# Optimization experiments

Measured on AMD Instinct MI355X. Metric: run time of the kernel, lower is better.

## Reference

```python
import jax, jax.numpy as jnp
import numpy as np

BN_EPS = 1e-5


def setup_inputs() -> dict:
    key = jax.random.key(0)
    k1, k2, k3 = jax.random.split(key, 3)
    B, IN, H, C = 65536, 784, 1024, 10
    x = jax.random.normal(k1, (B, IN), dtype=jnp.float32)
    # Kaiming-ish real-valued latent weights
    w1 = jax.random.normal(k2, (H, IN), dtype=jnp.float32) * 0.03
    w2 = jax.random.normal(k3, (C, H), dtype=jnp.float32) * 0.03
    gamma = jnp.ones((H,), dtype=jnp.float32)
    beta = jnp.zeros((H,), dtype=jnp.float32)
    return {"x": x, "w1": w1, "w2": w2, "gamma": gamma, "beta": beta}


def _bin_weight(w):
    # XNOR-Net weight binarization: per-output-row alpha * sign(w)
    alpha = jnp.mean(jnp.abs(w), axis=1, keepdims=True)  # [out, 1]
    return alpha * jnp.sign(w)


def reference(x, w1, w2, gamma, beta):
    x = x.reshape(x.shape[0], -1)                      # [B, 784]
    h = x @ _bin_weight(w1).T                          # [B, 1024]
    # BatchNorm1d, training mode: batch mean / biased variance
    mu = jnp.mean(h, axis=0)
    var = jnp.mean(jnp.square(h - mu), axis=0)
    h = gamma * (h - mu) * jax.lax.rsqrt(var + BN_EPS) + beta
    a = jnp.sign(h)                                    # binarized activation
    out = a @ _bin_weight(w2).T                        # [B, 10]
    return out
```

## Files before the change

### kernel.cpp

```cpp
#include <hip/hip_runtime.h>
#include <hip/hip_fp16.h>

#define BATCH   65536
#define IN_DIM  784
#define KPAD    800
#define K2      1600
#define KH      800
#define NSTEP   25
#define H_DIM   1024
#define C_DIM   10
#define BN_EPS  1e-5f

typedef _Float16 half8 __attribute__((ext_vector_type(8)));
typedef _Float16 half4 __attribute__((ext_vector_type(4)));
typedef float    f32x4 __attribute__((ext_vector_type(4)));

#if defined(__has_builtin)
#if __has_builtin(__builtin_amdgcn_global_load_lds)
#define HAVE_ASYNC 1
#endif
#endif
#ifndef HAVE_ASYNC
#define HAVE_ASYNC 0
#endif

__device__ __forceinline__ void stage16(const _Float16* g, _Float16* ldsBase, int lane) {
#if HAVE_ASYNC
  __builtin_amdgcn_global_load_lds((const __attribute__((address_space(1))) void*)g,
                                   (__attribute__((address_space(3))) void*)ldsBase,
                                   16, 0, 0);
#else
  *(half8*)(ldsBase + lane * 8) = *(const half8*)g;
#endif
}

__global__ __launch_bounds__(256) void split_x(const float* __restrict__ x,
                                               _Float16* __restrict__ X2) {
  const long tid = (long)blockIdx.x * 256 + threadIdx.x;
  const long row = tid / 100;
  const int  q   = (int)(tid - row * 100);
  const int  k   = q * 8;
  half8 hi = {}, lo = {};
  if (k < IN_DIM) {
#pragma unroll
    for (int h4 = 0; h4 < 2; ++h4) {
      const f32x4 v = *(const f32x4*)&x[row * IN_DIM + k + h4 * 4];
#pragma unroll
      for (int i = 0; i < 4; ++i) {
        const _Float16 h = (_Float16)v[i];
        hi[h4 * 4 + i] = h;
        lo[h4 * 4 + i] = (_Float16)(v[i] - (float)h);
      }
    }
  }
  _Float16* dst = X2 + row * K2 + k;
  *(half8*)dst = hi;
  *(half8*)(dst + KPAD) = lo;
}

__global__ __launch_bounds__(256) void prep_w(const float* __restrict__ w1,
                                              const float* __restrict__ w2,
                                              float* __restrict__ alpha1,
                                              _Float16* __restrict__ S2,
                                              float* __restrict__ bw2) {
  __shared__ float red[4];
  const int tid = threadIdx.x, lane = tid & 63, wave = tid >> 6;
  const int j = blockIdx.x;
  if (j < H_DIM) {
    const float* wr = w1 + (long)j * IN_DIM;
    float s = 0.f;
    for (int k = tid; k < IN_DIM; k += 256) s += fabsf(wr[k]);
#pragma unroll
    for (int off = 32; off > 0; off >>= 1) s += __shfl_xor(s, off, 64);
    if (lane == 0) red[wave] = s;
    __syncthreads();
    if (tid == 0) alpha1[j] = (red[0] + red[1] + red[2] + red[3]) * (1.f / IN_DIM);
    _Float16* dr = S2 + (long)j * KH;
    for (int k = tid; k < KH; k += 256) {
      const float v = (k < IN_DIM) ? wr[k] : 0.f;
      dr[k] = (_Float16)((v > 0.f) ? 1.f : ((v < 0.f) ? -1.f : 0.f));
    }
  } else {
    const int c = j - H_DIM;
    const float* wr = w2 + (long)c * H_DIM;
    float s = 0.f;
    for (int k = tid; k < H_DIM; k += 256) s += fabsf(wr[k]);
#pragma unroll
    for (int off = 32; off > 0; off >>= 1) s += __shfl_xor(s, off, 64);
    if (lane == 0) red[wave] = s;
    __syncthreads();
    const float alpha = (red[0] + red[1] + red[2] + red[3]) * (1.f / H_DIM);
    for (int k = tid; k < H_DIM; k += 256) {
      const float v = wr[k];
      const float sg = (v > 0.f) ? 1.f : ((v < 0.f) ? -1.f : 0.f);
      bw2[(long)c * H_DIM + k] = alpha * sg;
    }
  }
}

__global__ __launch_bounds__(512, 2) void gemm1(const _Float16* __restrict__ X2,
                                                const _Float16* __restrict__ S2,
                                                const float* __restrict__ alpha1,
                                                float* __restrict__ H,
                                                float* __restrict__ colsum,
                                                float* __restrict__ colsumsq) {
  __shared__ _Float16 lds[3 * 24576];
  const int tid  = threadIdx.x;
  const int lane = tid & 63;
  const int w    = tid >> 6;
  const int wr   = w >> 2;
  const int wc   = w & 3;

  const int b     = blockIdx.x;
  const int xcd   = b & 7;
  const int local = b >> 3;
  const long m0   = (long)(xcd * 32 + (local >> 2)) * 256;
  const int  n0   = (local & 3) * 256;

  const int c8 = ((lane & 3) ^ ((lane >> 3) & 3)) * 8;
  const _Float16* aG = X2 + (m0 + w * 32 + (lane >> 2)) * K2 + c8;
  const _Float16* bG = S2 + (long)(n0 + w * 32 + (lane >> 2)) * KH + c8;
  const int ldsW0 = (w * 32) * 32;
  const int ldsW1 = (w * 32 + 16) * 32;

  const int fr = lane & 15;
  const int kc = lane >> 4;
  const int cp = (kc ^ ((fr >> 1) & 3)) * 8;
  const int aoff = (wr * 128 + fr) * 32 + cp;
  const int boff = (wc * 64 + fr) * 32 + cp;

  f32x4 acc[8][4] = {};

#pragma unroll
  for (int kt = 0; kt < 2; ++kt) {
    _Float16* S = &lds[kt * 24576];
    const int k0 = kt * 32;
    stage16(aG + k0,                  S + ldsW0, lane);
    stage16(aG + 16 * K2 + k0,        S + ldsW1, lane);
    stage16(aG + KPAD + k0,           S + 8192 + ldsW0, lane);
    stage16(aG + KPAD + 16 * K2 + k0, S + 8192 + ldsW1, lane);
    stage16(bG + k0,                  S + 16384 + ldsW0, lane);
    stage16(bG + 16 * KH + k0,        S + 16384 + ldsW1, lane);
  }

  int scur = 0;
  int spre = 2;
  for (int t = 0; t < NSTEP; ++t) {
    _Float16* S = &lds[scur * 24576];
    const int ks = (t + 2 < NSTEP) ? (t + 2) * 32 : (NSTEP - 1) * 32;
    _Float16* P = &lds[spre * 24576];

    asm volatile("s_waitcnt vmcnt(6)" ::: "memory");
    __builtin_amdgcn_s_barrier();
    asm volatile("" ::: "memory");

    stage16(aG + ks,                  P + ldsW0, lane);
    stage16(aG + 16 * K2 + ks,        P + ldsW1, lane);
    stage16(aG + KPAD + ks,           P + 8192 + ldsW0, lane);
    stage16(aG + KPAD + 16 * K2 + ks, P + 8192 + ldsW1, lane);
    half8 af[8], bf[4];
#pragma unroll
    for (int ni = 0; ni < 4; ++ni) bf[ni] = *(const half8*)&S[16384 + boff + ni * 512];
#pragma unroll
    for (int mi = 0; mi < 8; ++mi) af[mi] = *(const half8*)&S[aoff + mi * 512];
    __builtin_amdgcn_s_setprio(1);
#pragma unroll
    for (int mi = 0; mi < 8; ++mi)
#pragma unroll
      for (int ni = 0; ni < 4; ++ni)
        acc[mi][ni] = __builtin_amdgcn_mfma_f32_16x16x32_f16(af[mi], bf[ni], acc[mi][ni], 0, 0, 0);
    __builtin_amdgcn_s_setprio(0);
    __builtin_amdgcn_s_barrier();

    stage16(bG + ks,           P + 16384 + ldsW0, lane);
    stage16(bG + 16 * KH + ks, P + 16384 + ldsW1, lane);
#pragma unroll
    for (int mi = 0; mi < 8; ++mi) af[mi] = *(const half8*)&S[8192 + aoff + mi * 512];
    __builtin_amdgcn_s_setprio(1);
#pragma unroll
    for (int mi = 0; mi < 8; ++mi)
#pragma unroll
      for (int ni = 0; ni < 4; ++ni)
        acc[mi][ni] = __builtin_amdgcn_mfma_f32_16x16x32_f16(af[mi], bf[ni], acc[mi][ni], 0, 0, 0);
    __builtin_amdgcn_s_setprio(0);

    scur = (scur == 2) ? 0 : scur + 1;
    spre = (spre == 2) ? 0 : spre + 1;
  }

  asm volatile("s_waitcnt vmcnt(0)" ::: "memory");

  const int rq = (lane >> 4) * 4;
#pragma unroll
  for (int ni = 0; ni < 4; ++ni) {
    const int col = n0 + wc * 64 + ni * 16 + fr;
    const float a1 = alpha1[col];
    float s = 0.f, q = 0.f;
#pragma unroll
    for (int mi = 0; mi < 8; ++mi) {
#pragma unroll
      for (int r = 0; r < 4; ++r) {
        const long row = m0 + wr * 128 + mi * 16 + rq + r;
        const float v = acc[mi][ni][r] * a1;
        H[row * H_DIM + col] = v;
        s += v;
        q += v * v;
      }
    }
    s += __shfl_xor(s, 16, 64);
    s += __shfl_xor(s, 32, 64);
    q += __shfl_xor(q, 16, 64);
    q += __shfl_xor(q, 32, 64);
    if ((lane >> 4) == 0) {
      atomicAdd(&colsum[col], s);
      atomicAdd(&colsumsq[col], q);
    }
  }
}

__global__ __launch_bounds__(256, 2) void final_k(const float* __restrict__ H,
                                                  const float* __restrict__ colsum,
                                                  const float* __restrict__ colsumsq,
                                                  const float* __restrict__ gamma,
                                                  const float* __restrict__ beta,
                                                  const float* __restrict__ bw2,
                                                  float* __restrict__ out) {
  const int tid = threadIdx.x, lane = tid & 63, wave = tid >> 6;
  f32x4 w2r[4][C_DIM];
  f32x4 csr[4], tsr[4];
#pragma unroll
  for (int c4 = 0; c4 < 4; ++c4) {
    const int col = c4 * 256 + lane * 4;
    const f32x4 s  = *(const f32x4*)&colsum[col];
    const f32x4 q  = *(const f32x4*)&colsumsq[col];
    const f32x4 g  = *(const f32x4*)&gamma[col];
    const f32x4 bt = *(const f32x4*)&beta[col];
    f32x4 c, t;
#pragma unroll
    for (int i = 0; i < 4; ++i) {
      const float mu  = s[i] * (1.f / BATCH);
      const float var = q[i] * (1.f / BATCH) - mu * mu;
      c[i] = g[i] * rsqrtf(var + BN_EPS);
      t[i] = bt[i] - c[i] * mu;
    }
    csr[c4] = c;
    tsr[c4] = t;
#pragma unroll
    for (int oc = 0; oc < C_DIM; ++oc)
      w2r[c4][oc] = *(const f32x4*)&bw2[oc * H_DIM + col];
  }

  const long wrow0 = ((long)blockIdx.x * 4 + wave) * 8;
#pragma unroll 1
  for (int r = 0; r < 8; ++r) {
    const long row = wrow0 + r;
    const float* hr = H + row * H_DIM;
    f32x4 h[4];
#pragma unroll
    for (int c4 = 0; c4 < 4; ++c4) h[c4] = *(const f32x4*)&hr[c4 * 256 + lane * 4];
    float p[C_DIM] = {};
#pragma unroll
    for (int c4 = 0; c4 < 4; ++c4) {
      f32x4 a;
#pragma unroll
      for (int i = 0; i < 4; ++i) {
        const float hv = h[c4][i] * csr[c4][i] + tsr[c4][i];
        a[i] = (hv > 0.f) ? 1.f : ((hv < 0.f) ? -1.f : 0.f);
      }
#pragma unroll
      for (int oc = 0; oc < C_DIM; ++oc) {
        const f32x4 wv = w2r[c4][oc];
        p[oc] += a[0] * wv[0] + a[1] * wv[1] + a[2] * wv[2] + a[3] * wv[3];
      }
    }
#pragma unroll
    for (int oc = 0; oc < C_DIM; ++oc) {
#pragma unroll
      for (int off = 32; off > 0; off >>= 1) p[oc] += __shfl_xor(p[oc], off, 64);
    }
    if (lane == 0) {
#pragma unroll
      for (int oc = 0; oc < C_DIM; ++oc) out[row * C_DIM + oc] = p[oc];
    }
  }
}

extern "C" void kernel_launch(void* const* d_in, const int* in_sizes, int n_in,
                              void* d_out, int out_size, void* d_ws, size_t ws_size,
                              hipStream_t stream) {
  const float* x     = (const float*)d_in[0];
  const float* w1    = (const float*)d_in[1];
  const float* w2    = (const float*)d_in[2];
  const float* gamma = (const float*)d_in[3];
  const float* beta  = (const float*)d_in[4];
  float* out = (float*)d_out;

  char* ws = (char*)d_ws;
  _Float16* X2     = (_Float16*)(ws + 0);
  float*    H      = (float*)  (ws + 209715200LL);
  _Float16* S2     = (_Float16*)(ws + 478150656LL);
  float*    BW2    = (float*)  (ws + 481427456LL);
  float*    ALPHA1 = (float*)  (ws + 481468416LL);
  float*    COLS   = (float*)  (ws + 481472512LL);
  float*    COLQ   = (float*)  (ws + 481476608LL);

  hipMemsetAsync(COLS, 0, 2 * H_DIM * sizeof(float), stream);
  split_x<<<(BATCH * 100) / 256, 256, 0, stream>>>(x, X2);
  prep_w<<<H_DIM + C_DIM, 256, 0, stream>>>(w1, w2, ALPHA1, S2, BW2);
  gemm1<<<1024, 512, 0, stream>>>(X2, S2, ALPHA1, H, COLS, COLQ);
  final_k<<<BATCH / 32, 256, 0, stream>>>(H, COLS, COLQ, gamma, beta, BW2, out);
}
```

Baseline: 606.5 us.

## Fuse fp16 hi/lo split of x into GEMM1 staging and drop memset launch

Removes the separate split_x kernel and its 200MB intermediate X2 buffer. GEMM1 now loads fp32 x directly, converts it to fp16 hi/lo pairs in registers and writes them into swizzled LDS, while still staging the weight tiles asynchronously. The column-sum zeroing moves into an extra prep_w block, which removes the memset. In exchange, the A-tile path now uses synchronous register loads plus conversion work inside the pipelined loop, with more VGPR pressure. The occupancy hint of 2 in launch_bounds is also dropped.

```diff
diff --git a/kernel.cpp b/kernel.cpp
--- a/kernel.cpp
+++ b/kernel.cpp
@@ -3,16 +3,14 @@
 
 #define BATCH   65536
 #define IN_DIM  784
-#define KPAD    800
-#define K2      1600
 #define KH      800
 #define NSTEP   25
 #define H_DIM   1024
 #define C_DIM   10
 #define BN_EPS  1e-5f
+#define SLOT    24576
 
 typedef _Float16 half8 __attribute__((ext_vector_type(8)));
-typedef _Float16 half4 __attribute__((ext_vector_type(4)));
 typedef float    f32x4 __attribute__((ext_vector_type(4)));
 
 #if defined(__has_builtin)
@@ -34,35 +32,12 @@
 #endif
 }
 
-__global__ __launch_bounds__(256) void split_x(const float* __restrict__ x,
-                                               _Float16* __restrict__ X2) {
-  const long tid = (long)blockIdx.x * 256 + threadIdx.x;
-  const long row = tid / 100;
-  const int  q   = (int)(tid - row * 100);
-  const int  k   = q * 8;
-  half8 hi = {}, lo = {};
-  if (k < IN_DIM) {
-#pragma unroll
-    for (int h4 = 0; h4 < 2; ++h4) {
-      const f32x4 v = *(const f32x4*)&x[row * IN_DIM + k + h4 * 4];
-#pragma unroll
-      for (int i = 0; i < 4; ++i) {
-        const _Float16 h = (_Float16)v[i];
-        hi[h4 * 4 + i] = h;
-        lo[h4 * 4 + i] = (_Float16)(v[i] - (float)h);
-      }
-    }
-  }
-  _Float16* dst = X2 + row * K2 + k;
-  *(half8*)dst = hi;
-  *(half8*)(dst + KPAD) = lo;
-}
-
 __global__ __launch_bounds__(256) void prep_w(const float* __restrict__ w1,
                                               const float* __restrict__ w2,
                                               float* __restrict__ alpha1,
                                               _Float16* __restrict__ S2,
-                                              float* __restrict__ bw2) {
+                                              float* __restrict__ bw2,
+                                              float* __restrict__ colz) {
   __shared__ float red[4];
   const int tid = threadIdx.x, lane = tid & 63, wave = tid >> 6;
   const int j = blockIdx.x;
@@ -80,7 +55,7 @@
       const float v = (k < IN_DIM) ? wr[k] : 0.f;
       dr[k] = (_Float16)((v > 0.f) ? 1.f : ((v < 0.f) ? -1.f : 0.f));
     }
-  } else {
+  } else if (j < H_DIM + C_DIM) {
     const int c = j - H_DIM;
     const float* wr = w2 + (long)c * H_DIM;
     float s = 0.f;
@@ -95,16 +70,18 @@
       const float sg = (v > 0.f) ? 1.f : ((v < 0.f) ? -1.f : 0.f);
       bw2[(long)c * H_DIM + k] = alpha * sg;
     }
-  }
-}
-
-__global__ __launch_bounds__(512, 2) void gemm1(const _Float16* __restrict__ X2,
-                                                const _Float16* __restrict__ S2,
-                                                const float* __restrict__ alpha1,
-                                                float* __restrict__ H,
-                                                float* __restrict__ colsum,
-                                                float* __restrict__ colsumsq) {
-  __shared__ _Float16 lds[3 * 24576];
+  } else {
+    for (int k = tid; k < 2 * H_DIM; k += 256) colz[k] = 0.f;
+  }
+}
+
+__global__ __launch_bounds__(512) void gemm1(const float* __restrict__ x,
+                                             const _Float16* __restrict__ S2,
+                                             const float* __restrict__ alpha1,
+                                             float* __restrict__ H,
+                                             float* __restrict__ colsum,
+                                             float* __restrict__ colsumsq) {
+  __shared__ _Float16 lds[3 * SLOT];
   const int tid  = threadIdx.x;
   const int lane = tid & 63;
   const int w    = tid >> 6;
@@ -117,8 +94,15 @@
   const long m0   = (long)(xcd * 32 + (local >> 2)) * 256;
   const int  n0   = (local & 3) * 256;
 
+  const int rowS  = tid >> 1;
+  const int halfS = tid & 1;
+  const float* xp = x + (m0 + rowS) * (long)IN_DIM;
+  const int sA = (rowS >> 1) & 3;
+  const int c0 = (halfS * 2) ^ sA;
+  const int c1 = (halfS * 2 + 1) ^ sA;
+  const int aw = rowS * 32;
+
   const int c8 = ((lane & 3) ^ ((lane >> 3) & 3)) * 8;
-  const _Float16* aG = X2 + (m0 + w * 32 + (lane >> 2)) * K2 + c8;
   const _Float16* bG = S2 + (long)(n0 + w * 32 + (lane >> 2)) * KH + c8;
   const int ldsW0 = (w * 32) * 32;
   const int ldsW1 = (w * 32 + 16) * 32;
@@ -133,31 +117,56 @@
 
 #pragma unroll
   for (int kt = 0; kt < 2; ++kt) {
-    _Float16* S = &lds[kt * 24576];
-    const int k0 = kt * 32;
-    stage16(aG + k0,                  S + ldsW0, lane);
-    stage16(aG + 16 * K2 + k0,        S + ldsW1, lane);
-    stage16(aG + KPAD + k0,           S + 8192 + ldsW0, lane);
-    stage16(aG + KPAD + 16 * K2 + k0, S + 8192 + ldsW1, lane);
-    stage16(bG + k0,                  S + 16384 + ldsW0, lane);
-    stage16(bG + 16 * KH + k0,        S + 16384 + ldsW1, lane);
-  }
+    _Float16* S = &lds[kt * SLOT];
+    const int ks = kt * 32;
+    const bool valid = (ks + halfS * 16) <= (IN_DIM - 16);
+    half8 hh0 = {}, hh1 = {}, hl0 = {}, hl1 = {};
+    if (valid) {
+      const float* src = xp + ks + halfS * 16;
+      f32x4 v0 = *(const f32x4*)(src);
+      f32x4 v1 = *(const f32x4*)(src + 4);
+      f32x4 v2 = *(const f32x4*)(src + 8);
+      f32x4 v3 = *(const f32x4*)(src + 12);
+#pragma unroll
+      for (int i = 0; i < 8; ++i) {
+        const float f0 = (i < 4) ? v0[i & 3] : v1[i & 3];
+        const float f1 = (i < 4) ? v2[i & 3] : v3[i & 3];
+        const _Float16 h0 = (_Float16)f0, h1 = (_Float16)f1;
+        hh0[i] = h0; hl0[i] = (_Float16)(f0 - (float)h0);
+        hh1[i] = h1; hl1[i] = (_Float16)(f1 - (float)h1);
+      }
+    }
+    *(half8*)(S + aw + c0 * 8) = hh0;
+    *(half8*)(S + aw + c1 * 8) = hh1;
+    *(half8*)(S + 8192 + aw + c0 * 8) = hl0;
+    *(half8*)(S + 8192 + aw + c1 * 8) = hl1;
+    stage16(bG + ks,           S + 16384 + ldsW0, lane);
+    stage16(bG + 16 * KH + ks, S + 16384 + ldsW1, lane);
+  }
+  asm volatile("s_waitcnt vmcnt(2) lgkmcnt(0)" ::: "memory");
 
   int scur = 0;
   int spre = 2;
   for (int t = 0; t < NSTEP; ++t) {
-    _Float16* S = &lds[scur * 24576];
-    const int ks = (t + 2 < NSTEP) ? (t + 2) * 32 : (NSTEP - 1) * 32;
-    _Float16* P = &lds[spre * 24576];
-
-    asm volatile("s_waitcnt vmcnt(6)" ::: "memory");
+    _Float16* S = &lds[scur * SLOT];
+    _Float16* P = &lds[spre * SLOT];
+    const int tcl = (t + 2 < NSTEP) ? (t + 2) : (NSTEP - 1);
+    const int ks = tcl * 32;
+    const bool validP = (ks + halfS * 16) <= (IN_DIM - 16);
+
+    asm volatile("" ::: "memory");
+    asm volatile("s_waitcnt vmcnt(2)" ::: "memory");
     __builtin_amdgcn_s_barrier();
     asm volatile("" ::: "memory");
 
-    stage16(aG + ks,                  P + ldsW0, lane);
-    stage16(aG + 16 * K2 + ks,        P + ldsW1, lane);
-    stage16(aG + KPAD + ks,           P + 8192 + ldsW0, lane);
-    stage16(aG + KPAD + 16 * K2 + ks, P + 8192 + ldsW1, lane);
+    f32x4 v0, v1, v2, v3;
+    if (validP) {
+      const float* src = xp + ks + halfS * 16;
+      v0 = *(const f32x4*)(src);
+      v1 = *(const f32x4*)(src + 4);
+      v2 = *(const f32x4*)(src + 8);
+      v3 = *(const f32x4*)(src + 12);
+    }
     half8 af[8], bf[4];
 #pragma unroll
     for (int ni = 0; ni < 4; ++ni) bf[ni] = *(const half8*)&S[16384 + boff + ni * 512];
@@ -170,8 +179,27 @@
       for (int ni = 0; ni < 4; ++ni)
         acc[mi][ni] = __builtin_amdgcn_mfma_f32_16x16x32_f16(af[mi], bf[ni], acc[mi][ni], 0, 0, 0);
     __builtin_amdgcn_s_setprio(0);
+    asm volatile("" ::: "memory");
     __builtin_amdgcn_s_barrier();
-
+    asm volatile("" ::: "memory");
+
+    {
+      half8 hh0 = {}, hh1 = {}, hl0 = {}, hl1 = {};
+      if (validP) {
+#pragma unroll
+        for (int i = 0; i < 8; ++i) {
+          const float f0 = (i < 4) ? v0[i & 3] : v1[i & 3];
+          const float f1 = (i < 4) ? v2[i & 3] : v3[i & 3];
+          const _Float16 h0 = (_Float16)f0, h1 = (_Float16)f1;
+          hh0[i] = h0; hl0[i] = (_Float16)(f0 - (float)h0);
+          hh1[i] = h1; hl1[i] = (_Float16)(f1 - (float)h1);
+        }
+      }
+      *(half8*)(P + aw + c0 * 8) = hh0;
+      *(half8*)(P + aw + c1 * 8) = hh1;
+      *(half8*)(P + 8192 + aw + c0 * 8) = hl0;
+      *(half8*)(P + 8192 + aw + c1 * 8) = hl1;
+    }
     stage16(bG + ks,           P + 16384 + ldsW0, lane);
     stage16(bG + 16 * KH + ks, P + 16384 + ldsW1, lane);
 #pragma unroll
@@ -296,17 +324,14 @@
   float* out = (float*)d_out;
 
   char* ws = (char*)d_ws;
-  _Float16* X2     = (_Float16*)(ws + 0);
-  float*    H      = (float*)  (ws + 209715200LL);
-  _Float16* S2     = (_Float16*)(ws + 478150656LL);
-  float*    BW2    = (float*)  (ws + 481427456LL);
-  float*    ALPHA1 = (float*)  (ws + 481468416LL);
-  float*    COLS   = (float*)  (ws + 481472512LL);
-  float*    COLQ   = (float*)  (ws + 481476608LL);
-
-  hipMemsetAsync(COLS, 0, 2 * H_DIM * sizeof(float), stream);
-  split_x<<<(BATCH * 100) / 256, 256, 0, stream>>>(x, X2);
-  prep_w<<<H_DIM + C_DIM, 256, 0, stream>>>(w1, w2, ALPHA1, S2, BW2);
-  gemm1<<<1024, 512, 0, stream>>>(X2, S2, ALPHA1, H, COLS, COLQ);
+  float*    H      = (float*)  (ws + 0);
+  _Float16* S2     = (_Float16*)(ws + 268435456LL);
+  float*    BW2    = (float*)  (ws + 270073856LL);
+  float*    ALPHA1 = (float*)  (ws + 270114816LL);
+  float*    COLS   = (float*)  (ws + 270118912LL);
+  float*    COLQ   = (float*)  (ws + 270123008LL);
+
+  prep_w<<<H_DIM + C_DIM + 1, 256, 0, stream>>>(w1, w2, ALPHA1, S2, BW2, COLS);
+  gemm1<<<1024, 512, 0, stream>>>(x, S2, ALPHA1, H, COLS, COLQ);
   final_k<<<BATCH / 32, 256, 0, stream>>>(H, COLS, COLQ, gamma, beta, BW2, out);
 }
```

Result: faster. 586.2 us (-3.3%).
